# Optimization experiments

Measured on AMD Instinct MI355X. Metric: run time of the kernel, lower is better.

The kernel has to match this reference:

```python
import jax, jax.numpy as jnp
import numpy as np

DIM = 1024
N_QUAT = DIM // 4
LN_EPS = 1e-5
NORM_EPS = 1e-12


def quat_mul(q1, q2):
    # q1, q2: [B, L, N, 4]
    r1, i1, j1, k1 = q1[..., 0], q1[..., 1], q1[..., 2], q1[..., 3]
    r2, i2, j2, k2 = q2[..., 0], q2[..., 1], q2[..., 2], q2[..., 3]
    r = r1 * r2 - i1 * i2 - j1 * j2 - k1 * k2
    i = r1 * i2 + i1 * r2 + j1 * k2 - k1 * j2
    j = r1 * j2 - i1 * k2 + j1 * r2 + k1 * i2
    k = r1 * k2 + i1 * j2 - j1 * i2 + k1 * r2
    return jnp.stack([r, i, j, k], axis=-1)


def quat_conj(q):
    return q * jnp.array([1.0, -1.0, -1.0, -1.0], dtype=q.dtype)


def setup_inputs() -> dict:
    key = jax.random.key(0)
    ks = jax.random.split(key, 7)
    B, L, D = 4, 4096, DIM
    s = 1.0 / np.sqrt(D)
    return {
        "x": jax.random.normal(ks[0], (B, L, D), dtype=jnp.float32),
        "Wk": jax.random.normal(ks[1], (D, D), dtype=jnp.float32) * s,
        "bk": jnp.zeros((D,), dtype=jnp.float32),
        "Wv": jax.random.normal(ks[2], (D, D), dtype=jnp.float32) * s,
        "bv": jnp.zeros((D,), dtype=jnp.float32),
        "ln_g": jnp.ones((D,), dtype=jnp.float32),
        "ln_b": jnp.zeros((D,), dtype=jnp.float32),
        "Wo": jax.random.normal(ks[3], (D, D), dtype=jnp.float32) * s,
        "bo": jnp.zeros((D,), dtype=jnp.float32),
    }


def reference(x, Wk, bk, Wv, bv, ln_g, ln_b, Wo, bo):
    B, L, D = x.shape
    keys = (x @ Wk.T + bk).reshape(B, L, N_QUAT, 4)
    knorm = jnp.linalg.norm(keys, axis=-1, keepdims=True)
    keys = keys / jnp.maximum(knorm, NORM_EPS)  # F.normalize
    values = (x @ Wv.T + bv).reshape(B, L, N_QUAT, 4)
    bound = quat_mul(values, keys)
    memory = jnp.cumsum(bound, axis=1)
    retrieved = quat_mul(memory, quat_conj(keys)).reshape(B, L, D)
    positions = jnp.arange(1, L + 1, dtype=x.dtype)
    retrieved = retrieved / jnp.sqrt(positions)[None, :, None]
    # LayerNorm over last dim
    mu = jnp.mean(retrieved, axis=-1, keepdims=True)
    var = jnp.var(retrieved, axis=-1, keepdims=True)
    normed = (retrieved - mu) / jnp.sqrt(var + LN_EPS) * ln_g + ln_b
    return x + (normed @ Wo.T + bo)
```

## Files before the change

### kernel.cpp

```cpp
#include <hip/hip_runtime.h>
#include <cstdint>
#include <cstddef>


typedef float    f32x4 __attribute__((ext_vector_type(4)));
typedef _Float16 f16x8 __attribute__((ext_vector_type(8)));
typedef _Float16 f16x4 __attribute__((ext_vector_type(4)));

#define DEV static __device__ __forceinline__

constexpr int BATCH = 4;
constexpr int LSEQ  = 4096;
constexpr int DIMN  = 1024;
constexpr int MROW  = BATCH * LSEQ;
constexpr int SEG   = 64;
constexpr int SL    = LSEQ / SEG;
constexpr int NT    = DIMN / 64;

DEV f32x4 qmul(f32x4 a, f32x4 b) {
  f32x4 r;
  r.x = a.x*b.x - a.y*b.y - a.z*b.z - a.w*b.w;
  r.y = a.x*b.y + a.y*b.x + a.z*b.w - a.w*b.z;
  r.z = a.x*b.z - a.y*b.w + a.z*b.x + a.w*b.y;
  r.w = a.x*b.w + a.y*b.z - a.z*b.y + a.w*b.x;
  return r;
}

__global__ __launch_bounds__(256) void k_cast_f16(const float* __restrict__ in,
                                                  _Float16* __restrict__ out, int n4) {
  int i = blockIdx.x * 256 + threadIdx.x;
  if (i < n4) {
    f32x4 v = ((const f32x4*)in)[i];
    f16x4 o = { (_Float16)v.x, (_Float16)v.y, (_Float16)v.z, (_Float16)v.w };
    ((f16x4*)out)[i] = o;
  }
}

__global__ __launch_bounds__(512, 2) void k_gemm256(
    const _Float16* __restrict__ A, const _Float16* __restrict__ Bw,
    const float* __restrict__ biasA, const float* __restrict__ biasB, int nsplit,
    const float* __restrict__ resid, float* __restrict__ C, int ldC, int nbn) {
  extern __shared__ char smem[];
  const int tid  = threadIdx.x;
  const int lane = tid & 63;
  const int wid  = tid >> 6;
  const int wr = wid >> 2, wc = wid & 3;

  const int nwg = gridDim.x;
  const int cpx = nwg >> 3;
  const int swz = (blockIdx.x & 7) * cpx + (blockIdx.x >> 3);
  const int bm = swz / nbn, bn = swz % nbn;

  auto regBase = [](int slot, int isB, int half) -> unsigned {
    return (unsigned)(((slot * 2 + isB) * 2 + half) * 16384);
  };
  const int r8    = lane >> 3;
  const int sslot = (lane & 7) ^ r8;
  const char* aT = (const char*)(A  + (size_t)bm * 256 * DIMN);
  const char* bT = (const char*)(Bw + (size_t)bn * 256 * DIMN);

  auto stage = [&](int isB, int half, int slot, int kt) {
    const char* gb = (isB ? bT : aT) + (size_t)(half * 128) * 2048 + kt * 128;
    const unsigned reg = regBase(slot, isB, half);
#pragma unroll
    for (int i = 0; i < 2; ++i) {
      const int c = wid * 2 + i;
      const char* src = gb + (size_t)(c * 8 + r8) * 2048 + (sslot << 4);
      __builtin_amdgcn_global_load_lds(
          (const __attribute__((address_space(1))) void*)src,
          (__attribute__((address_space(3))) void*)(smem + reg + c * 1024), 16, 0, 0);
    }
  };
  auto fragA = [&](int slot, int m, int kk) -> f16x8 {
    const int half = m >> 2;
    const int row  = wr * 64 + (m & 3) * 16 + (lane & 15);
    const int sl   = (kk * 4 + (lane >> 4)) ^ (row & 7);
    return *(const f16x8*)(smem + regBase(slot, 0, half) + row * 128 + (sl << 4));
  };
  auto fragB = [&](int slot, int n, int kk) -> f16x8 {
    const int half = n >> 1;
    const int row  = wc * 32 + (n & 1) * 16 + (lane & 15);
    const int sl   = (kk * 4 + (lane >> 4)) ^ (row & 7);
    return *(const f16x8*)(smem + regBase(slot, 1, half) + row * 128 + (sl << 4));
  };

  f32x4 acc[8][4];
#pragma unroll
  for (int m = 0; m < 8; ++m)
#pragma unroll
    for (int n = 0; n < 4; ++n) acc[m][n] = (f32x4){0.f, 0.f, 0.f, 0.f};

  stage(0, 0, 0, 0); stage(1, 0, 0, 0); stage(0, 1, 0, 0); stage(1, 1, 0, 0);
  asm volatile("s_waitcnt vmcnt(4)" ::: "memory");
  __builtin_amdgcn_s_barrier();

  f16x8 a[4][2], b0[2][2], b1[2][2];
#pragma unroll 2
  for (int T = 0; T < NT; ++T) {
    const int slot = T & 1, ns = slot ^ 1;
    const bool pf = (T + 1 < NT);
#pragma unroll
    for (int m = 0; m < 4; ++m) { a[m][0] = fragA(slot, m, 0); a[m][1] = fragA(slot, m, 1); }
#pragma unroll
    for (int n = 0; n < 2; ++n) { b0[n][0] = fragB(slot, n, 0); b0[n][1] = fragB(slot, n, 1); }
    if (pf) stage(0, 0, ns, T + 1);
    asm volatile("s_waitcnt vmcnt(2)" ::: "memory");
    __builtin_amdgcn_s_barrier();
    __builtin_amdgcn_s_setprio(1);
#pragma unroll
    for (int m = 0; m < 4; ++m)
#pragma unroll
      for (int n = 0; n < 2; ++n) {
        acc[m][n] = __builtin_amdgcn_mfma_f32_16x16x32_f16(a[m][0], b0[n][0], acc[m][n], 0, 0, 0);
        acc[m][n] = __builtin_amdgcn_mfma_f32_16x16x32_f16(a[m][1], b0[n][1], acc[m][n], 0, 0, 0);
      }
    __builtin_amdgcn_s_setprio(0);
    __builtin_amdgcn_s_barrier();
#pragma unroll
    for (int n = 0; n < 2; ++n) { b1[n][0] = fragB(slot, n + 2, 0); b1[n][1] = fragB(slot, n + 2, 1); }
    if (pf) stage(1, 0, ns, T + 1);
    __builtin_amdgcn_s_barrier();
    __builtin_amdgcn_s_setprio(1);
#pragma unroll
    for (int m = 0; m < 4; ++m)
#pragma unroll
      for (int n = 0; n < 2; ++n) {
        acc[m][n + 2] = __builtin_amdgcn_mfma_f32_16x16x32_f16(a[m][0], b1[n][0], acc[m][n + 2], 0, 0, 0);
        acc[m][n + 2] = __builtin_amdgcn_mfma_f32_16x16x32_f16(a[m][1], b1[n][1], acc[m][n + 2], 0, 0, 0);
      }
    __builtin_amdgcn_s_setprio(0);
    __builtin_amdgcn_s_barrier();
#pragma unroll
    for (int m = 0; m < 4; ++m) { a[m][0] = fragA(slot, m + 4, 0); a[m][1] = fragA(slot, m + 4, 1); }
    if (pf) stage(0, 1, ns, T + 1);
    __builtin_amdgcn_s_barrier();
    __builtin_amdgcn_s_setprio(1);
#pragma unroll
    for (int m = 0; m < 4; ++m)
#pragma unroll
      for (int n = 0; n < 2; ++n) {
        acc[m + 4][n] = __builtin_amdgcn_mfma_f32_16x16x32_f16(a[m][0], b0[n][0], acc[m + 4][n], 0, 0, 0);
        acc[m + 4][n] = __builtin_amdgcn_mfma_f32_16x16x32_f16(a[m][1], b0[n][1], acc[m + 4][n], 0, 0, 0);
      }
    __builtin_amdgcn_s_setprio(0);
    __builtin_amdgcn_s_barrier();
    if (pf) stage(1, 1, ns, T + 1);
    asm volatile("s_waitcnt vmcnt(4)" ::: "memory");
    __builtin_amdgcn_s_barrier();
    __builtin_amdgcn_s_setprio(1);
#pragma unroll
    for (int m = 0; m < 4; ++m)
#pragma unroll
      for (int n = 0; n < 2; ++n) {
        acc[m + 4][n + 2] = __builtin_amdgcn_mfma_f32_16x16x32_f16(a[m][0], b1[n][0], acc[m + 4][n + 2], 0, 0, 0);
        acc[m + 4][n + 2] = __builtin_amdgcn_mfma_f32_16x16x32_f16(a[m][1], b1[n][1], acc[m + 4][n + 2], 0, 0, 0);
      }
    __builtin_amdgcn_s_setprio(0);
    __builtin_amdgcn_s_barrier();
  }

  const int r0 = bm * 256 + wr * 64 + ((lane >> 4) << 2);
  const int c0 = bn * 256 + wc * 32 + (lane & 15);
#pragma unroll
  for (int n = 0; n < 4; ++n) {
    const int col = c0 + (n >> 1) * 128 + (n & 1) * 16;
    const float bc = (col < nsplit) ? biasA[col] : biasB[col - nsplit];
#pragma unroll
    for (int m = 0; m < 8; ++m) {
      const int row = r0 + (m >> 2) * 128 + (m & 3) * 16;
#pragma unroll
      for (int t = 0; t < 4; ++t) {
        const size_t off = (size_t)(row + t) * ldC + col;
        float v = acc[m][n][t] + bc;
        if (resid) v += resid[(size_t)(row + t) * DIMN + col];
        C[off] = v;
      }
    }
  }
}

__global__ __launch_bounds__(512, 2) void k_gemm128(
    const _Float16* __restrict__ A, const _Float16* __restrict__ Bw,
    const float* __restrict__ bias, const float* __restrict__ resid,
    float* __restrict__ C, int nbn) {
  extern __shared__ char smem[];
  const int tid  = threadIdx.x;
  const int lane = tid & 63;
  const int wid  = tid >> 6;
  const int wr = wid >> 2, wc = wid & 3;

  const int nwg = gridDim.x;
  const int cpx = nwg >> 3;
  const int swz = (blockIdx.x & 7) * cpx + (blockIdx.x >> 3);
  const int bm = swz / nbn, bn = swz % nbn;

  const int r8    = lane >> 3;
  const int sslot = (lane & 7) ^ r8;
  const char* aT = (const char*)(A  + (size_t)bm * 128 * DIMN);
  const char* bT = (const char*)(Bw + (size_t)bn * 256 * DIMN);

  auto stageA = [&](int slot, int kt) {
    const char* gb = aT + kt * 128;
    char* dst = smem + slot * 16384;
#pragma unroll
    for (int i = 0; i < 2; ++i) {
      const int c = wid * 2 + i;
      const char* src = gb + (size_t)(c * 8 + r8) * 2048 + (sslot << 4);
      __builtin_amdgcn_global_load_lds(
          (const __attribute__((address_space(1))) void*)src,
          (__attribute__((address_space(3))) void*)(dst + c * 1024), 16, 0, 0);
    }
  };
  auto stageB = [&](int slot, int half, int kt) {
    const char* gb = bT + (size_t)(half * 128) * 2048 + kt * 128;
    char* dst = smem + 32768 + (slot * 2 + half) * 16384;
#pragma unroll
    for (int i = 0; i < 2; ++i) {
      const int c = wid * 2 + i;
      const char* src = gb + (size_t)(c * 8 + r8) * 2048 + (sslot << 4);
      __builtin_amdgcn_global_load_lds(
          (const __attribute__((address_space(1))) void*)src,
          (__attribute__((address_space(3))) void*)(dst + c * 1024), 16, 0, 0);
    }
  };
  auto fragA = [&](int slot, int m, int kk) -> f16x8 {
    const int row = wr * 64 + m * 16 + (lane & 15);
    const int sl  = (kk * 4 + (lane >> 4)) ^ (row & 7);
    return *(const f16x8*)(smem + slot * 16384 + row * 128 + (sl << 4));
  };
  auto fragB = [&](int slot, int n, int kk) -> f16x8 {
    const int half = n >> 1;
    const int lrow = wc * 32 + (n & 1) * 16 + (lane & 15);
    const int sl   = (kk * 4 + (lane >> 4)) ^ (lrow & 7);
    return *(const f16x8*)(smem + 32768 + (slot * 2 + half) * 16384 + lrow * 128 + (sl << 4));
  };

  f32x4 acc[4][4];
#pragma unroll
  for (int m = 0; m < 4; ++m)
#pragma unroll
    for (int n = 0; n < 4; ++n) acc[m][n] = (f32x4){0.f, 0.f, 0.f, 0.f};

  stageA(0, 0); stageB(0, 0, 0); stageB(0, 1, 0);
  asm volatile("s_waitcnt vmcnt(2)" ::: "memory");
  __builtin_amdgcn_s_barrier();

  f16x8 a[4][2], b0[2][2], b1[2][2];
#pragma unroll 2
  for (int T = 0; T < NT; ++T) {
    const int slot = T & 1, ns = slot ^ 1;
    const bool pf = (T + 1 < NT);
#pragma unroll
    for (int m = 0; m < 4; ++m) { a[m][0] = fragA(slot, m, 0); a[m][1] = fragA(slot, m, 1); }
#pragma unroll
    for (int n = 0; n < 2; ++n) { b0[n][0] = fragB(slot, n, 0); b0[n][1] = fragB(slot, n, 1); }
    if (pf) {
      stageA(ns, T + 1); stageB(ns, 0, T + 1);
      asm volatile("s_waitcnt vmcnt(4)" ::: "memory");
    } else {
      asm volatile("s_waitcnt vmcnt(0)" ::: "memory");
    }
    __builtin_amdgcn_s_barrier();
    __builtin_amdgcn_s_setprio(1);
#pragma unroll
    for (int m = 0; m < 4; ++m)
#pragma unroll
      for (int n = 0; n < 2; ++n) {
        acc[m][n] = __builtin_amdgcn_mfma_f32_16x16x32_f16(a[m][0], b0[n][0], acc[m][n], 0, 0, 0);
        acc[m][n] = __builtin_amdgcn_mfma_f32_16x16x32_f16(a[m][1], b0[n][1], acc[m][n], 0, 0, 0);
      }
    __builtin_amdgcn_s_setprio(0);
    __builtin_amdgcn_s_barrier();
#pragma unroll
    for (int n = 0; n < 2; ++n) { b1[n][0] = fragB(slot, n + 2, 0); b1[n][1] = fragB(slot, n + 2, 1); }
    if (pf) {
      stageB(ns, 1, T + 1);
      asm volatile("s_waitcnt vmcnt(2)" ::: "memory");
    }
    __builtin_amdgcn_s_barrier();
    __builtin_amdgcn_s_setprio(1);
#pragma unroll
    for (int m = 0; m < 4; ++m)
#pragma unroll
      for (int n = 0; n < 2; ++n) {
        acc[m][n + 2] = __builtin_amdgcn_mfma_f32_16x16x32_f16(a[m][0], b1[n][0], acc[m][n + 2], 0, 0, 0);
        acc[m][n + 2] = __builtin_amdgcn_mfma_f32_16x16x32_f16(a[m][1], b1[n][1], acc[m][n + 2], 0, 0, 0);
      }
    __builtin_amdgcn_s_setprio(0);
    __builtin_amdgcn_s_barrier();
  }

  const int r0 = bm * 128 + wr * 64 + ((lane >> 4) << 2);
  const int c0 = bn * 256 + wc * 32 + (lane & 15);
#pragma unroll
  for (int n = 0; n < 4; ++n) {
    const int col = c0 + (n >> 1) * 128 + (n & 1) * 16;
    const float bc = bias[col];
#pragma unroll
    for (int m = 0; m < 4; ++m) {
      const int row = r0 + m * 16;
#pragma unroll
      for (int t = 0; t < 4; ++t) {
        const size_t off = (size_t)(row + t) * DIMN + col;
        C[off] = acc[m][n][t] + bc + resid[off];
      }
    }
  }
}

__global__ __launch_bounds__(256) void k_segsum(const float* __restrict__ KV,
                                                float* __restrict__ segsum) {
  const int b = blockIdx.x >> 6, seg = blockIdx.x & 63, n = threadIdx.x;
  f32x4 ssum = (f32x4){0.f, 0.f, 0.f, 0.f};
  const size_t rb = (size_t)(b * LSEQ + seg * SL) * 2048 + n * 4;
  for (int l = 0; l < SL; ++l) {
    const size_t p = rb + (size_t)l * 2048;
    f32x4 kq = *(const f32x4*)(KV + p);
    f32x4 vq = *(const f32x4*)(KV + p + 1024);
    float nn = sqrtf(kq.x*kq.x + kq.y*kq.y + kq.z*kq.z + kq.w*kq.w);
    f32x4 kh = kq * (1.0f / fmaxf(nn, 1e-12f));
    ssum += qmul(vq, kh);
  }
  ((f32x4*)segsum)[(size_t)blockIdx.x * 256 + n] = ssum;
}

__global__ __launch_bounds__(256) void k_segscan(const float* __restrict__ segsum,
                                                 float* __restrict__ segoff) {
  const int gt = blockIdx.x * 256 + threadIdx.x;
  const int b = gt >> 10, ch = gt & 1023;
  float run = 0.f;
  for (int s = 0; s < SEG; ++s) {
    const size_t idx = ((size_t)(b * SEG + s)) * 1024 + ch;
    float v = segsum[idx];
    segoff[idx] = run;
    run += v;
  }
}

__global__ __launch_bounds__(256) void k_retrieve_ln(
    const float* __restrict__ KV, const float* __restrict__ segoff,
    const float* __restrict__ g, const float* __restrict__ bb,
    _Float16* __restrict__ out) {
  const int b = blockIdx.x >> 6, seg = blockIdx.x & 63, n = threadIdx.x;
  const int wid = n >> 6, lane = n & 63;
  __shared__ float p1[2][4], p2[2][4];
  f32x4 mem = ((const f32x4*)segoff)[(size_t)blockIdx.x * 256 + n];
  const f32x4 gg  = ((const f32x4*)g)[n];
  const f32x4 bvv = ((const f32x4*)bb)[n];
  const size_t rb = (size_t)(b * LSEQ + seg * SL) * 2048 + n * 4;
  const int grow = b * LSEQ + seg * SL;

  f32x4 kq = *(const f32x4*)(KV + rb);
  f32x4 vq = *(const f32x4*)(KV + rb + 1024);
  for (int l = 0; l < SL; ++l) {
    f32x4 kqn, vqn;
    if (l + 1 < SL) {
      kqn = *(const f32x4*)(KV + rb + (size_t)(l + 1) * 2048);
      vqn = *(const f32x4*)(KV + rb + (size_t)(l + 1) * 2048 + 1024);
    }
    float nn = sqrtf(kq.x*kq.x + kq.y*kq.y + kq.z*kq.z + kq.w*kq.w);
    f32x4 kh = kq * (1.0f / fmaxf(nn, 1e-12f));
    mem += qmul(vq, kh);
    f32x4 kc = (f32x4){kh.x, -kh.y, -kh.z, -kh.w};
    f32x4 r = qmul(mem, kc);
    r *= rsqrtf((float)(seg * SL + l + 1));

    float s1 = r.x + r.y + r.z + r.w;
    float s2 = r.x*r.x + r.y*r.y + r.z*r.z + r.w*r.w;
#pragma unroll
    for (int off = 32; off > 0; off >>= 1) {
      s1 += __shfl_down(s1, off, 64);
      s2 += __shfl_down(s2, off, 64);
    }
    if (lane == 0) { p1[l & 1][wid] = s1; p2[l & 1][wid] = s2; }
    __syncthreads();
    const float ts1 = p1[l & 1][0] + p1[l & 1][1] + p1[l & 1][2] + p1[l & 1][3];
    const float ts2 = p2[l & 1][0] + p2[l & 1][1] + p2[l & 1][2] + p2[l & 1][3];
    const float mu = ts1 * (1.0f / 1024.0f);
    const float var = ts2 * (1.0f / 1024.0f) - mu * mu;
    const float rstd = rsqrtf(var + 1e-5f);
    f32x4 nv = (r - mu) * rstd * gg + bvv;
    f16x4 o = { (_Float16)nv.x, (_Float16)nv.y, (_Float16)nv.z, (_Float16)nv.w };
    ((f16x4*)out)[(size_t)(grow + l) * 256 + n] = o;
    kq = kqn; vq = vqn;
  }
}

extern "C" void kernel_launch(void* const* d_in, const int* in_sizes, int n_in,
                              void* d_out, int out_size, void* d_ws, size_t ws_size,
                              hipStream_t stream) {
  const float* x    = (const float*)d_in[0];
  const float* Wk   = (const float*)d_in[1];
  const float* bk   = (const float*)d_in[2];
  const float* Wv   = (const float*)d_in[3];
  const float* bv   = (const float*)d_in[4];
  const float* ln_g = (const float*)d_in[5];
  const float* ln_b = (const float*)d_in[6];
  const float* Wo   = (const float*)d_in[7];
  const float* bo   = (const float*)d_in[8];
  float* out = (float*)d_out;

  char* ws = (char*)d_ws;
  size_t off = 0;
  auto alloc = [&](size_t bytes) -> void* {
    void* p = ws + off;
    off += (bytes + 255) & ~(size_t)255;
    return p;
  };
  _Float16* xb   = (_Float16*)alloc((size_t)MROW * DIMN * 2);
  _Float16* wkvb = (_Float16*)alloc((size_t)2 * DIMN * DIMN * 2);
  _Float16* wob  = (_Float16*)alloc((size_t)DIMN * DIMN * 2);
  float* KV      = (float*)alloc((size_t)MROW * 2 * DIMN * 4);
  float* segsum  = (float*)alloc((size_t)BATCH * SEG * DIMN * 4);
  float* segoff  = (float*)alloc((size_t)BATCH * SEG * DIMN * 4);
  _Float16* nb   = (_Float16*)alloc((size_t)MROW * DIMN * 2);
  (void)off; (void)ws_size; (void)in_sizes; (void)n_in; (void)out_size;

  hipFuncSetAttribute((const void*)k_gemm256,
                      hipFuncAttributeMaxDynamicSharedMemorySize, 131072);
  hipFuncSetAttribute((const void*)k_gemm128,
                      hipFuncAttributeMaxDynamicSharedMemorySize, 98304);

  k_cast_f16<<<MROW * DIMN / 4 / 256, 256, 0, stream>>>(x, xb, MROW * DIMN / 4);
  k_cast_f16<<<DIMN * DIMN / 4 / 256, 256, 0, stream>>>(Wk, wkvb, DIMN * DIMN / 4);
  k_cast_f16<<<DIMN * DIMN / 4 / 256, 256, 0, stream>>>(Wv, wkvb + (size_t)DIMN * DIMN, DIMN * DIMN / 4);
  k_cast_f16<<<DIMN * DIMN / 4 / 256, 256, 0, stream>>>(Wo, wob, DIMN * DIMN / 4);

  k_gemm256<<<(MROW / 256) * (2048 / 256), 512, 131072, stream>>>(
      xb, wkvb, bk, bv, 1024, nullptr, KV, 2048, 2048 / 256);

  k_segsum<<<BATCH * SEG, 256, 0, stream>>>(KV, segsum);
  k_segscan<<<BATCH * DIMN / 256, 256, 0, stream>>>(segsum, segoff);
  k_retrieve_ln<<<BATCH * SEG, 256, 0, stream>>>(KV, segoff, ln_g, ln_b, nb);

  k_gemm128<<<(MROW / 128) * (DIMN / 256), 512, 98304, stream>>>(
      nb, wob, bo, x, out, DIMN / 256);
}
```

Measured before the change: 256.7 us.

## Store KV in fp16, triple-buffer output GEMM, fuse weight casts, double segments

The KV projection output is written as fp16, and the scan/retrieve kernels read and widen it, halving the intermediate memory traffic. The output GEMM now uses a three-stage LDS pipeline with a single combined A/B staging, and it reads the residual from the fp16 copy of x. The three weight casts are merged into one launch, the KV GEMM issues all prefetches at the top of each iteration, and the segment count is doubled for more parallelism. The cost is reduced precision in K/V and in the residual add.

```diff
diff --git a/kernel.cpp b/kernel.cpp
--- a/kernel.cpp
+++ b/kernel.cpp
@@ -13,7 +13,7 @@
 constexpr int LSEQ  = 4096;
 constexpr int DIMN  = 1024;
 constexpr int MROW  = BATCH * LSEQ;
-constexpr int SEG   = 64;
+constexpr int SEG   = 128;
 constexpr int SL    = LSEQ / SEG;
 constexpr int NT    = DIMN / 64;
 
@@ -26,6 +26,10 @@
   return r;
 }
 
+DEV f32x4 h2f(f16x4 h) {
+  return (f32x4){(float)h.x, (float)h.y, (float)h.z, (float)h.w};
+}
+
 __global__ __launch_bounds__(256) void k_cast_f16(const float* __restrict__ in,
                                                   _Float16* __restrict__ out, int n4) {
   int i = blockIdx.x * 256 + threadIdx.x;
@@ -36,10 +40,23 @@
   }
 }
 
+__global__ __launch_bounds__(256) void k_cast_w3(const float* __restrict__ w0,
+                                                 const float* __restrict__ w1,
+                                                 const float* __restrict__ w2,
+                                                 _Float16* __restrict__ out, int n4each) {
+  int i = blockIdx.x * 256 + threadIdx.x;
+  if (i >= 3 * n4each) return;
+  const float* src = (i < n4each) ? w0 : (i < 2 * n4each ? w1 : w2);
+  int j = (i < n4each) ? i : (i < 2 * n4each ? i - n4each : i - 2 * n4each);
+  f32x4 v = ((const f32x4*)src)[j];
+  f16x4 o = { (_Float16)v.x, (_Float16)v.y, (_Float16)v.z, (_Float16)v.w };
+  ((f16x4*)out)[i] = o;
+}
+
 __global__ __launch_bounds__(512, 2) void k_gemm256(
     const _Float16* __restrict__ A, const _Float16* __restrict__ Bw,
     const float* __restrict__ biasA, const float* __restrict__ biasB, int nsplit,
-    const float* __restrict__ resid, float* __restrict__ C, int ldC, int nbn) {
+    _Float16* __restrict__ C, int ldC, int nbn) {
   extern __shared__ char smem[];
   const int tid  = threadIdx.x;
   const int lane = tid & 63;
@@ -99,12 +116,16 @@
   for (int T = 0; T < NT; ++T) {
     const int slot = T & 1, ns = slot ^ 1;
     const bool pf = (T + 1 < NT);
+    if (pf) {
+      stage(0, 0, ns, T + 1); stage(1, 0, ns, T + 1);
+      stage(0, 1, ns, T + 1); stage(1, 1, ns, T + 1);
+    }
 #pragma unroll
     for (int m = 0; m < 4; ++m) { a[m][0] = fragA(slot, m, 0); a[m][1] = fragA(slot, m, 1); }
 #pragma unroll
     for (int n = 0; n < 2; ++n) { b0[n][0] = fragB(slot, n, 0); b0[n][1] = fragB(slot, n, 1); }
-    if (pf) stage(0, 0, ns, T + 1);
-    asm volatile("s_waitcnt vmcnt(2)" ::: "memory");
+    if (pf) asm volatile("s_waitcnt vmcnt(8)" ::: "memory");
+    else    asm volatile("s_waitcnt vmcnt(0)" ::: "memory");
     __builtin_amdgcn_s_barrier();
     __builtin_amdgcn_s_setprio(1);
 #pragma unroll
@@ -118,7 +139,6 @@
     __builtin_amdgcn_s_barrier();
 #pragma unroll
     for (int n = 0; n < 2; ++n) { b1[n][0] = fragB(slot, n + 2, 0); b1[n][1] = fragB(slot, n + 2, 1); }
-    if (pf) stage(1, 0, ns, T + 1);
     __builtin_amdgcn_s_barrier();
     __builtin_amdgcn_s_setprio(1);
 #pragma unroll
@@ -132,7 +152,6 @@
     __builtin_amdgcn_s_barrier();
 #pragma unroll
     for (int m = 0; m < 4; ++m) { a[m][0] = fragA(slot, m + 4, 0); a[m][1] = fragA(slot, m + 4, 1); }
-    if (pf) stage(0, 1, ns, T + 1);
     __builtin_amdgcn_s_barrier();
     __builtin_amdgcn_s_setprio(1);
 #pragma unroll
@@ -144,8 +163,7 @@
       }
     __builtin_amdgcn_s_setprio(0);
     __builtin_amdgcn_s_barrier();
-    if (pf) stage(1, 1, ns, T + 1);
-    asm volatile("s_waitcnt vmcnt(4)" ::: "memory");
+    if (pf) asm volatile("s_waitcnt vmcnt(4)" ::: "memory");
     __builtin_amdgcn_s_barrier();
     __builtin_amdgcn_s_setprio(1);
 #pragma unroll
@@ -170,18 +188,15 @@
       const int row = r0 + (m >> 2) * 128 + (m & 3) * 16;
 #pragma unroll
       for (int t = 0; t < 4; ++t) {
-        const size_t off = (size_t)(row + t) * ldC + col;
-        float v = acc[m][n][t] + bc;
-        if (resid) v += resid[(size_t)(row + t) * DIMN + col];
-        C[off] = v;
-      }
-    }
-  }
-}
-
-__global__ __launch_bounds__(512, 2) void k_gemm128(
+        C[(size_t)(row + t) * ldC + col] = (_Float16)(acc[m][n][t] + bc);
+      }
+    }
+  }
+}
+
+__global__ __launch_bounds__(512, 2) void k_gemm_out(
     const _Float16* __restrict__ A, const _Float16* __restrict__ Bw,
-    const float* __restrict__ bias, const float* __restrict__ resid,
+    const float* __restrict__ bias, const _Float16* __restrict__ residH,
     float* __restrict__ C, int nbn) {
   extern __shared__ char smem[];
   const int tid  = threadIdx.x;
@@ -199,40 +214,34 @@
   const char* aT = (const char*)(A  + (size_t)bm * 128 * DIMN);
   const char* bT = (const char*)(Bw + (size_t)bn * 256 * DIMN);
 
-  auto stageA = [&](int slot, int kt) {
-    const char* gb = aT + kt * 128;
-    char* dst = smem + slot * 16384;
+  auto stage3 = [&](int slot, int kt) {
+    char* base = smem + slot * 49152;
 #pragma unroll
     for (int i = 0; i < 2; ++i) {
       const int c = wid * 2 + i;
-      const char* src = gb + (size_t)(c * 8 + r8) * 2048 + (sslot << 4);
+      const char* src = aT + kt * 128 + (size_t)(c * 8 + r8) * 2048 + (sslot << 4);
       __builtin_amdgcn_global_load_lds(
           (const __attribute__((address_space(1))) void*)src,
-          (__attribute__((address_space(3))) void*)(dst + c * 1024), 16, 0, 0);
-    }
-  };
-  auto stageB = [&](int slot, int half, int kt) {
-    const char* gb = bT + (size_t)(half * 128) * 2048 + kt * 128;
-    char* dst = smem + 32768 + (slot * 2 + half) * 16384;
-#pragma unroll
-    for (int i = 0; i < 2; ++i) {
-      const int c = wid * 2 + i;
-      const char* src = gb + (size_t)(c * 8 + r8) * 2048 + (sslot << 4);
+          (__attribute__((address_space(3))) void*)(base + c * 1024), 16, 0, 0);
+    }
+#pragma unroll
+    for (int i = 0; i < 4; ++i) {
+      const int c = wid * 4 + i;
+      const char* src = bT + kt * 128 + (size_t)(c * 8 + r8) * 2048 + (sslot << 4);
       __builtin_amdgcn_global_load_lds(
           (const __attribute__((address_space(1))) void*)src,
-          (__attribute__((address_space(3))) void*)(dst + c * 1024), 16, 0, 0);
+          (__attribute__((address_space(3))) void*)(base + 16384 + c * 1024), 16, 0, 0);
     }
   };
   auto fragA = [&](int slot, int m, int kk) -> f16x8 {
     const int row = wr * 64 + m * 16 + (lane & 15);
     const int sl  = (kk * 4 + (lane >> 4)) ^ (row & 7);
-    return *(const f16x8*)(smem + slot * 16384 + row * 128 + (sl << 4));
+    return *(const f16x8*)(smem + slot * 49152 + row * 128 + (sl << 4));
   };
   auto fragB = [&](int slot, int n, int kk) -> f16x8 {
-    const int half = n >> 1;
-    const int lrow = wc * 32 + (n & 1) * 16 + (lane & 15);
-    const int sl   = (kk * 4 + (lane >> 4)) ^ (lrow & 7);
-    return *(const f16x8*)(smem + 32768 + (slot * 2 + half) * 16384 + lrow * 128 + (sl << 4));
+    const int row = (n >> 1) * 128 + wc * 32 + (n & 1) * 16 + (lane & 15);
+    const int sl  = (kk * 4 + (lane >> 4)) ^ (row & 7);
+    return *(const f16x8*)(smem + slot * 49152 + 16384 + row * 128 + (sl << 4));
   };
 
   f32x4 acc[4][4];
@@ -241,25 +250,19 @@
 #pragma unroll
     for (int n = 0; n < 4; ++n) acc[m][n] = (f32x4){0.f, 0.f, 0.f, 0.f};
 
-  stageA(0, 0); stageB(0, 0, 0); stageB(0, 1, 0);
-  asm volatile("s_waitcnt vmcnt(2)" ::: "memory");
+  stage3(0, 0); stage3(1, 1);
+  asm volatile("s_waitcnt vmcnt(6)" ::: "memory");
   __builtin_amdgcn_s_barrier();
 
   f16x8 a[4][2], b0[2][2], b1[2][2];
 #pragma unroll 2
   for (int T = 0; T < NT; ++T) {
-    const int slot = T & 1, ns = slot ^ 1;
-    const bool pf = (T + 1 < NT);
-#pragma unroll
-    for (int m = 0; m < 4; ++m) { a[m][0] = fragA(slot, m, 0); a[m][1] = fragA(slot, m, 1); }
-#pragma unroll
-    for (int n = 0; n < 2; ++n) { b0[n][0] = fragB(slot, n, 0); b0[n][1] = fragB(slot, n, 1); }
-    if (pf) {
-      stageA(ns, T + 1); stageB(ns, 0, T + 1);
-      asm volatile("s_waitcnt vmcnt(4)" ::: "memory");
-    } else {
-      asm volatile("s_waitcnt vmcnt(0)" ::: "memory");
-    }
+    const int s = T % 3, sw = (T + 2) % 3;
+    if (T + 2 < NT) stage3(sw, T + 2);
+#pragma unroll
+    for (int m = 0; m < 4; ++m) { a[m][0] = fragA(s, m, 0); a[m][1] = fragA(s, m, 1); }
+#pragma unroll
+    for (int n = 0; n < 2; ++n) { b0[n][0] = fragB(s, n, 0); b0[n][1] = fragB(s, n, 1); }
     __builtin_amdgcn_s_barrier();
     __builtin_amdgcn_s_setprio(1);
 #pragma unroll
@@ -272,11 +275,9 @@
     __builtin_amdgcn_s_setprio(0);
     __builtin_amdgcn_s_barrier();
 #pragma unroll
-    for (int n = 0; n < 2; ++n) { b1[n][0] = fragB(slot, n + 2, 0); b1[n][1] = fragB(slot, n + 2, 1); }
-    if (pf) {
-      stageB(ns, 1, T + 1);
-      asm volatile("s_waitcnt vmcnt(2)" ::: "memory");
-    }
+    for (int n = 0; n < 2; ++n) { b1[n][0] = fragB(s, n + 2, 0); b1[n][1] = fragB(s, n + 2, 1); }
+    if (T < NT - 2)       asm volatile("s_waitcnt vmcnt(6)" ::: "memory");
+    else if (T == NT - 2) asm volatile("s_waitcnt vmcnt(0)" ::: "memory");
     __builtin_amdgcn_s_barrier();
     __builtin_amdgcn_s_setprio(1);
 #pragma unroll
@@ -302,21 +303,21 @@
 #pragma unroll
       for (int t = 0; t < 4; ++t) {
         const size_t off = (size_t)(row + t) * DIMN + col;
-        C[off] = acc[m][n][t] + bc + resid[off];
-      }
-    }
-  }
-}
-
-__global__ __launch_bounds__(256) void k_segsum(const float* __restrict__ KV,
+        C[off] = acc[m][n][t] + bc + (float)residH[off];
+      }
+    }
+  }
+}
+
+__global__ __launch_bounds__(256) void k_segsum(const _Float16* __restrict__ KVh,
                                                 float* __restrict__ segsum) {
-  const int b = blockIdx.x >> 6, seg = blockIdx.x & 63, n = threadIdx.x;
+  const int b = blockIdx.x >> 7, seg = blockIdx.x & 127, n = threadIdx.x;
   f32x4 ssum = (f32x4){0.f, 0.f, 0.f, 0.f};
   const size_t rb = (size_t)(b * LSEQ + seg * SL) * 2048 + n * 4;
   for (int l = 0; l < SL; ++l) {
     const size_t p = rb + (size_t)l * 2048;
-    f32x4 kq = *(const f32x4*)(KV + p);
-    f32x4 vq = *(const f32x4*)(KV + p + 1024);
+    f32x4 kq = h2f(*(const f16x4*)(KVh + p));
+    f32x4 vq = h2f(*(const f16x4*)(KVh + p + 1024));
     float nn = sqrtf(kq.x*kq.x + kq.y*kq.y + kq.z*kq.z + kq.w*kq.w);
     f32x4 kh = kq * (1.0f / fmaxf(nn, 1e-12f));
     ssum += qmul(vq, kh);
@@ -338,10 +339,10 @@
 }
 
 __global__ __launch_bounds__(256) void k_retrieve_ln(
-    const float* __restrict__ KV, const float* __restrict__ segoff,
+    const _Float16* __restrict__ KVh, const float* __restrict__ segoff,
     const float* __restrict__ g, const float* __restrict__ bb,
     _Float16* __restrict__ out) {
-  const int b = blockIdx.x >> 6, seg = blockIdx.x & 63, n = threadIdx.x;
+  const int b = blockIdx.x >> 7, seg = blockIdx.x & 127, n = threadIdx.x;
   const int wid = n >> 6, lane = n & 63;
   __shared__ float p1[2][4], p2[2][4];
   f32x4 mem = ((const f32x4*)segoff)[(size_t)blockIdx.x * 256 + n];
@@ -350,17 +351,18 @@
   const size_t rb = (size_t)(b * LSEQ + seg * SL) * 2048 + n * 4;
   const int grow = b * LSEQ + seg * SL;
 
-  f32x4 kq = *(const f32x4*)(KV + rb);
-  f32x4 vq = *(const f32x4*)(KV + rb + 1024);
+  f16x4 kq = *(const f16x4*)(KVh + rb);
+  f16x4 vq = *(const f16x4*)(KVh + rb + 1024);
   for (int l = 0; l < SL; ++l) {
-    f32x4 kqn, vqn;
+    f16x4 kqn, vqn;
     if (l + 1 < SL) {
-      kqn = *(const f32x4*)(KV + rb + (size_t)(l + 1) * 2048);
-      vqn = *(const f32x4*)(KV + rb + (size_t)(l + 1) * 2048 + 1024);
-    }
-    float nn = sqrtf(kq.x*kq.x + kq.y*kq.y + kq.z*kq.z + kq.w*kq.w);
-    f32x4 kh = kq * (1.0f / fmaxf(nn, 1e-12f));
-    mem += qmul(vq, kh);
+      kqn = *(const f16x4*)(KVh + rb + (size_t)(l + 1) * 2048);
+      vqn = *(const f16x4*)(KVh + rb + (size_t)(l + 1) * 2048 + 1024);
+    }
+    f32x4 kf = h2f(kq), vf = h2f(vq);
+    float nn = sqrtf(kf.x*kf.x + kf.y*kf.y + kf.z*kf.z + kf.w*kf.w);
+    f32x4 kh = kf * (1.0f / fmaxf(nn, 1e-12f));
+    mem += qmul(vf, kh);
     f32x4 kc = (f32x4){kh.x, -kh.y, -kh.z, -kh.w};
     f32x4 r = qmul(mem, kc);
     r *= rsqrtf((float)(seg * SL + l + 1));
@@ -408,31 +410,29 @@
     return p;
   };
   _Float16* xb   = (_Float16*)alloc((size_t)MROW * DIMN * 2);
-  _Float16* wkvb = (_Float16*)alloc((size_t)2 * DIMN * DIMN * 2);
-  _Float16* wob  = (_Float16*)alloc((size_t)DIMN * DIMN * 2);
-  float* KV      = (float*)alloc((size_t)MROW * 2 * DIMN * 4);
+  _Float16* wkvb = (_Float16*)alloc((size_t)3 * DIMN * DIMN * 2);
+  _Float16* KVh  = (_Float16*)alloc((size_t)MROW * 2 * DIMN * 2);
   float* segsum  = (float*)alloc((size_t)BATCH * SEG * DIMN * 4);
   float* segoff  = (float*)alloc((size_t)BATCH * SEG * DIMN * 4);
   _Float16* nb   = (_Float16*)alloc((size_t)MROW * DIMN * 2);
+  _Float16* wob  = wkvb + (size_t)2 * DIMN * DIMN;
   (void)off; (void)ws_size; (void)in_sizes; (void)n_in; (void)out_size;
 
   hipFuncSetAttribute((const void*)k_gemm256,
                       hipFuncAttributeMaxDynamicSharedMemorySize, 131072);
-  hipFuncSetAttribute((const void*)k_gemm128,
-                      hipFuncAttributeMaxDynamicSharedMemorySize, 98304);
+  hipFuncSetAttribute((const void*)k_gemm_out,
+                      hipFuncAttributeMaxDynamicSharedMemorySize, 147456);
 
   k_cast_f16<<<MROW * DIMN / 4 / 256, 256, 0, stream>>>(x, xb, MROW * DIMN / 4);
-  k_cast_f16<<<DIMN * DIMN / 4 / 256, 256, 0, stream>>>(Wk, wkvb, DIMN * DIMN / 4);
-  k_cast_f16<<<DIMN * DIMN / 4 / 256, 256, 0, stream>>>(Wv, wkvb + (size_t)DIMN * DIMN, DIMN * DIMN / 4);
-  k_cast_f16<<<DIMN * DIMN / 4 / 256, 256, 0, stream>>>(Wo, wob, DIMN * DIMN / 4);
+  k_cast_w3<<<3 * DIMN * DIMN / 4 / 256, 256, 0, stream>>>(Wk, Wv, Wo, wkvb, DIMN * DIMN / 4);
 
   k_gemm256<<<(MROW / 256) * (2048 / 256), 512, 131072, stream>>>(
-      xb, wkvb, bk, bv, 1024, nullptr, KV, 2048, 2048 / 256);
-
-  k_segsum<<<BATCH * SEG, 256, 0, stream>>>(KV, segsum);
+      xb, wkvb, bk, bv, 1024, KVh, 2048, 2048 / 256);
+
+  k_segsum<<<BATCH * SEG, 256, 0, stream>>>(KVh, segsum);
   k_segscan<<<BATCH * DIMN / 256, 256, 0, stream>>>(segsum, segoff);
-  k_retrieve_ln<<<BATCH * SEG, 256, 0, stream>>>(KV, segoff, ln_g, ln_b, nb);
-
-  k_gemm128<<<(MROW / 128) * (DIMN / 256), 512, 98304, stream>>>(
-      nb, wob, bo, x, out, DIMN / 256);
-}
+  k_retrieve_ln<<<BATCH * SEG, 256, 0, stream>>>(KVh, segoff, ln_g, ln_b, nb);
+
+  k_gemm_out<<<(MROW / 128) * (DIMN / 256), 512, 147456, stream>>>(
+      nb, wob, bo, xb, out, DIMN / 256);
+}
```

Measured after the change: 207.2 us. 19.3% less time.
